# Kernel tuning notes

Measured on AMD Instinct MI355X. Metric: run time of the kernel, lower is better.

The kernel has to match this reference:

```python
import jax, jax.numpy as jnp
import numpy as np

N_NODES = 50000
N_EDGES = 800000
IN_DIM = 256
HID = 64
HEADS = 4
NUM_GRAPHS = 8
NEG_SLOPE = 0.2  # PyG GATConv default


def setup_inputs() -> dict:
    key = jax.random.key(0)
    ks = jax.random.split(key, 14)
    x = jax.random.normal(ks[0], (N_NODES, IN_DIM), jnp.float32)
    edge_index = jax.random.randint(ks[1], (2, N_EDGES), 0, N_NODES, jnp.int32)
    batch = jnp.sort(jax.random.randint(ks[2], (N_NODES,), 0, NUM_GRAPHS, jnp.int32))
    s1 = 1.0 / np.sqrt(IN_DIM)
    s2 = 1.0 / np.sqrt(HID * HEADS)
    W1 = jax.random.normal(ks[3], (IN_DIM, HEADS * HID), jnp.float32) * s1
    a_src1 = jax.random.normal(ks[4], (HEADS, HID), jnp.float32) * (1.0 / np.sqrt(HID))
    a_dst1 = jax.random.normal(ks[5], (HEADS, HID), jnp.float32) * (1.0 / np.sqrt(HID))
    b1 = jnp.zeros((HEADS * HID,), jnp.float32)
    W2 = jax.random.normal(ks[6], (HEADS * HID, HID), jnp.float32) * s2
    a_src2 = jax.random.normal(ks[7], (1, HID), jnp.float32) * (1.0 / np.sqrt(HID))
    a_dst2 = jax.random.normal(ks[8], (1, HID), jnp.float32) * (1.0 / np.sqrt(HID))
    b2 = jnp.zeros((HID,), jnp.float32)
    fcW = jax.random.normal(ks[9], (HID, 2), jnp.float32) * (1.0 / np.sqrt(HID))
    fcb = jnp.zeros((2,), jnp.float32)
    return {"x": x, "edge_index": edge_index, "batch": batch,
            "W1": W1, "a_src1": a_src1, "a_dst1": a_dst1, "b1": b1,
            "W2": W2, "a_src2": a_src2, "a_dst2": a_dst2, "b2": b2,
            "fcW": fcW, "fcb": fcb}


def _gat_layer(x, src, dst, W, a_src, a_dst, b, heads, out_dim, concat):
    """PyG-style GATConv: gather -> edge attention -> segment softmax -> scatter-add."""
    N = x.shape[0]
    xw = (x @ W).reshape(N, heads, out_dim)          # [N,H,C]
    al = jnp.einsum('nhc,hc->nh', xw, a_src)         # alpha_src per node
    ar = jnp.einsum('nhc,hc->nh', xw, a_dst)         # alpha_dst per node
    e = jax.nn.leaky_relu(al[src] + ar[dst], NEG_SLOPE)  # [E,H]
    m = jax.ops.segment_max(e, dst, num_segments=N)      # stable softmax per dst
    w = jnp.exp(e - m[dst])
    denom = jax.ops.segment_sum(w, dst, num_segments=N)
    alpha = w / denom[dst]                               # [E,H]
    out = jax.ops.segment_sum(alpha[:, :, None] * xw[src], dst, num_segments=N)  # [N,H,C]
    out = out.reshape(N, heads * out_dim) if concat else out.mean(axis=1)
    return out + b


def reference(x, edge_index, batch, W1, a_src1, a_dst1, b1, W2, a_src2, a_dst2, b2, fcW, fcb):
    N = x.shape[0]
    loops = jnp.arange(N, dtype=edge_index.dtype)  # PyG add_self_loops=True default
    src = jnp.concatenate([edge_index[0], loops])
    dst = jnp.concatenate([edge_index[1], loops])
    h = jax.nn.elu(_gat_layer(x, src, dst, W1, a_src1, a_dst1, b1, HEADS, HID, True))
    h = jax.nn.elu(_gat_layer(h, src, dst, W2, a_src2, a_dst2, b2, 1, HID, True))
    ssum = jax.ops.segment_sum(h, batch, num_segments=NUM_GRAPHS)
    cnt = jax.ops.segment_sum(jnp.ones((N, 1), h.dtype), batch, num_segments=NUM_GRAPHS)
    pooled = ssum / jnp.maximum(cnt, 1.0)  # global_mean_pool
    logits = pooled @ fcW + fcb
    return (h, logits)
```

## Files before the change

kernel.cpp:

```cpp
#include <hip/hip_runtime.h>

#define NEG_SLOPE 0.2f
#define NG 8
#define CH 64

typedef unsigned short ushort_t;
typedef __attribute__((ext_vector_type(8))) short short8v;
typedef __attribute__((ext_vector_type(4))) float f32x4;

__device__ __forceinline__ float lrelu(float x) { return x > 0.f ? x : NEG_SLOPE * x; }
__device__ __forceinline__ float eluf(float x) { return x > 0.f ? x : expm1f(x); }
__device__ __forceinline__ float wave_sum(float v) {
    #pragma unroll
    for (int o = 32; o; o >>= 1) v += __shfl_xor(v, o);
    return v;
}
__device__ __forceinline__ ushort_t f2bf(float f) {
    unsigned u = __float_as_uint(f);
    unsigned r = (u + 0x7FFFu + ((u >> 16) & 1u)) >> 16;
    return (ushort_t)r;
}
__device__ __forceinline__ float bf2f(ushort_t s) {
    return __uint_as_float(((unsigned)s) << 16);
}

__global__ __launch_bounds__(256) void k_hist(const int* __restrict__ ei,
                                              int* __restrict__ deg, int E) {
    int e = blockIdx.x * 256 + threadIdx.x;
    if (e < E) atomicAdd(&deg[ei[E + e]], 1);
}

__global__ __launch_bounds__(256) void k_scanA(const int* __restrict__ deg,
                                               int* __restrict__ bsum, int N) {
    __shared__ int wsums[4];
    int b = blockIdx.x, t = threadIdx.x;
    int base = b * 1024 + t * 4;
    int s = 0;
    #pragma unroll
    for (int k = 0; k < 4; k++) { int i = base + k; if (i < N) s += deg[i]; }
    #pragma unroll
    for (int o = 32; o; o >>= 1) s += __shfl_xor(s, o);
    if ((t & 63) == 0) wsums[t >> 6] = s;
    __syncthreads();
    if (t == 0) bsum[b] = wsums[0] + wsums[1] + wsums[2] + wsums[3];
}

__global__ __launch_bounds__(64) void k_scanB(const int* __restrict__ bsum,
                                              int* __restrict__ boff,
                                              int* __restrict__ rpN, int SB) {
    int lane = threadIdx.x;
    int own = (lane < SB) ? bsum[lane] : 0;
    int v = own;
    #pragma unroll
    for (int o = 1; o < 64; o <<= 1) { int y = __shfl_up(v, o); if (lane >= o) v += y; }
    if (lane < SB) boff[lane] = v - own;
    if (lane == 63) *rpN = v;
}

__global__ __launch_bounds__(256) void k_scanC(const int* __restrict__ deg,
                                               const int* __restrict__ boff,
                                               int* __restrict__ rp,
                                               int* __restrict__ cur, int N) {
    __shared__ int wtot[4];
    int b = blockIdx.x, t = threadIdx.x;
    int wid = t >> 6, lane = t & 63;
    int base = b * 1024 + t * 4;
    int d[4];
    #pragma unroll
    for (int k = 0; k < 4; k++) d[k] = (base + k < N) ? deg[base + k] : 0;
    int tsum = d[0] + d[1] + d[2] + d[3];
    int v = tsum;
    #pragma unroll
    for (int o = 1; o < 64; o <<= 1) { int y = __shfl_up(v, o); if (lane >= o) v += y; }
    if (lane == 63) wtot[wid] = v;
    __syncthreads();
    int wbase = 0;
    for (int k = 0; k < wid; k++) wbase += wtot[k];
    int run = boff[b] + wbase + v - tsum;
    #pragma unroll
    for (int k = 0; k < 4; k++) {
        if (base + k < N) { rp[base + k] = run; cur[base + k] = run; }
        run += d[k];
    }
}

__global__ __launch_bounds__(256) void k_fill(const int* __restrict__ ei,
                                              int* __restrict__ cur,
                                              int* __restrict__ csr, int E) {
    int e = blockIdx.x * 256 + threadIdx.x;
    if (e >= E) return;
    int s = ei[e], d = ei[E + e];
    int pos = atomicAdd(&cur[d], 1);
    csr[pos] = s;
}

__global__ __launch_bounds__(256) void k_w1t(const float* __restrict__ W1,
                                             ushort_t* __restrict__ w1th,
                                             ushort_t* __restrict__ w1tl) {
    int tile = blockIdx.x >> 3, ks = blockIdx.x & 7;
    for (int i = threadIdx.x; i < 512; i += 256) {
        int lane = i >> 3, e = i & 7;
        int jl = lane & 15, q = lane >> 4;
        int col = tile * 16 + jl;
        int k = ks * 32 + 8 * q + e;
        float w = W1[(size_t)k * 256 + col];
        ushort_t hi = f2bf(w);
        float lo = w - bf2f(hi);
        size_t o = (size_t)blockIdx.x * 512 + i;
        w1th[o] = hi;
        w1tl[o] = f2bf(lo);
    }
}

__global__ __launch_bounds__(256, 4) void k_gemm1(const float* __restrict__ x,
                                               const ushort_t* __restrict__ w1th,
                                               const ushort_t* __restrict__ w1tl,
                                               const float* __restrict__ a_s,
                                               const float* __restrict__ a_d,
                                               ushort_t* __restrict__ xw1b,
                                               float* __restrict__ al4,
                                               float* __restrict__ ar4, int N) {
    __shared__ __align__(16) unsigned char smem[33792];
    ushort_t* xh = (ushort_t*)smem;
    ushort_t* xl = (ushort_t*)(smem + 16896);
    int r0 = blockIdx.x * 32;
    int tid = threadIdx.x;
    int lane = tid & 63, wv = tid >> 6;
    for (int i = tid; i < 2048; i += 256) {
        int r = i >> 6, k4 = (i & 63) << 2;
        float4 v = (r0 + r < N) ? *(const float4*)(x + (size_t)(r0 + r) * 256 + k4)
                                : make_float4(0.f, 0.f, 0.f, 0.f);
        ushort4 h4, l4;
        h4.x = f2bf(v.x); l4.x = f2bf(v.x - bf2f(h4.x));
        h4.y = f2bf(v.y); l4.y = f2bf(v.y - bf2f(h4.y));
        h4.z = f2bf(v.z); l4.z = f2bf(v.z - bf2f(h4.z));
        h4.w = f2bf(v.w); l4.w = f2bf(v.w - bf2f(h4.w));
        *(ushort4*)(&xh[r * 264 + k4]) = h4;
        *(ushort4*)(&xl[r * 264 + k4]) = l4;
    }
    __syncthreads();
    int wr = wv & 1, wc = wv >> 1;
    int jl = lane & 15, q = lane >> 4;
    f32x4 acc[8];
    #pragma unroll
    for (int t = 0; t < 8; t++) acc[t] = (f32x4){0.f, 0.f, 0.f, 0.f};
    const ushort_t* xhp = &xh[(16 * wr + jl) * 264];
    const ushort_t* xlp = &xl[(16 * wr + jl) * 264];
    const ushort_t* bhb = w1th + (size_t)wc * 32768 + lane * 8;
    const ushort_t* blb = w1tl + (size_t)wc * 32768 + lane * 8;
    #pragma unroll 1
    for (int ks = 0; ks < 8; ks++) {
        int ko = 32 * ks + 8 * q;
        short8v ah = *(const short8v*)(xhp + ko);
        short8v alo = *(const short8v*)(xlp + ko);
        #pragma unroll
        for (int tp = 0; tp < 4; tp++) {
            int t0 = 2 * tp, t1 = 2 * tp + 1;
            short8v bh0 = *(const short8v*)(bhb + (t0 * 8 + ks) * 512);
            short8v bl0 = *(const short8v*)(blb + (t0 * 8 + ks) * 512);
            short8v bh1 = *(const short8v*)(bhb + (t1 * 8 + ks) * 512);
            short8v bl1 = *(const short8v*)(blb + (t1 * 8 + ks) * 512);
            acc[t0] = __builtin_amdgcn_mfma_f32_16x16x32_bf16(ah, bh0, acc[t0], 0, 0, 0);
            acc[t0] = __builtin_amdgcn_mfma_f32_16x16x32_bf16(ah, bl0, acc[t0], 0, 0, 0);
            acc[t0] = __builtin_amdgcn_mfma_f32_16x16x32_bf16(alo, bh0, acc[t0], 0, 0, 0);
            acc[t1] = __builtin_amdgcn_mfma_f32_16x16x32_bf16(ah, bh1, acc[t1], 0, 0, 0);
            acc[t1] = __builtin_amdgcn_mfma_f32_16x16x32_bf16(ah, bl1, acc[t1], 0, 0, 0);
            acc[t1] = __builtin_amdgcn_mfma_f32_16x16x32_bf16(alo, bh1, acc[t1], 0, 0, 0);
        }
    }
    __syncthreads();
    float* outb = (float*)smem;
    #pragma unroll
    for (int t = 0; t < 8; t++) {
        int c = 128 * wc + 16 * t + jl;
        int rb = 16 * wr + 4 * q;
        outb[(rb + 0) * 256 + c] = acc[t].x;
        outb[(rb + 1) * 256 + c] = acc[t].y;
        outb[(rb + 2) * 256 + c] = acc[t].z;
        outb[(rb + 3) * 256 + c] = acc[t].w;
    }
    __syncthreads();
    int c4 = lane << 2;
    int h = lane >> 4, kk = c4 & 63;
    float4 s4 = *(const float4*)(a_s + h * 64 + kk);
    float4 d4 = *(const float4*)(a_d + h * 64 + kk);
    float4 hv[8];
    #pragma unroll
    for (int t2 = 0; t2 < 8; t2++)
        hv[t2] = *(const float4*)(&outb[(wv + 4 * t2) * 256 + c4]);
    #pragma unroll
    for (int t2 = 0; t2 < 8; t2++) {
        float sl = hv[t2].x * s4.x + hv[t2].y * s4.y + hv[t2].z * s4.z + hv[t2].w * s4.w;
        float sr = hv[t2].x * d4.x + hv[t2].y * d4.y + hv[t2].z * d4.z + hv[t2].w * d4.w;
        #pragma unroll
        for (int o = 1; o < 16; o <<= 1) { sl += __shfl_xor(sl, o); sr += __shfl_xor(sr, o); }
        int r = r0 + wv + 4 * t2;
        if ((lane & 15) == 0 && r < N) {
            al4[(size_t)r * 4 + h] = sl;
            ar4[(size_t)r * 4 + h] = sr;
        }
    }
    __syncthreads();
    ushort_t* Ls = (ushort_t*)smem;
    #pragma unroll
    for (int t2 = 0; t2 < 8; t2++) {
        int rl = wv + 4 * t2;
        Ls[rl * 256 + (kk + 0) * 4 + h] = f2bf(hv[t2].x);
        Ls[rl * 256 + (kk + 1) * 4 + h] = f2bf(hv[t2].y);
        Ls[rl * 256 + (kk + 2) * 4 + h] = f2bf(hv[t2].z);
        Ls[rl * 256 + (kk + 3) * 4 + h] = f2bf(hv[t2].w);
    }
    __syncthreads();
    #pragma unroll
    for (int p = 0; p < 4; p++) {
        int flat = p * 2048 + tid * 8;
        int rl = flat >> 8, col = flat & 255;
        int r = r0 + rl;
        if (r < N)
            *(uint4*)(xw1b + (size_t)r * 256 + col) = *(const uint4*)(Ls + flat);
    }
}

__device__ __forceinline__ float4 wexp4(float4 a, float4 arn) {
    float4 w;
    w.x = __expf(lrelu(a.x + arn.x));
    w.y = __expf(lrelu(a.y + arn.y));
    w.z = __expf(lrelu(a.z + arn.z));
    w.w = __expf(lrelu(a.w + arn.w));
    return w;
}

__device__ __forceinline__ void gather1(int n, int lane,
                                        const int* __restrict__ rp,
                                        const int* __restrict__ csr,
                                        const float* __restrict__ al4,
                                        const float* __restrict__ ar4,
                                        const ushort_t* __restrict__ xw1b,
                                        const float* __restrict__ b1,
                                        float4* __restrict__ wb,
                                        int* __restrict__ sb,
                                        float* __restrict__ hrow) {
    int e0 = rp[n], e1 = rp[n + 1];
    float4 arn = *(const float4*)(ar4 + (size_t)n * 4);
    float4 aln = *(const float4*)(al4 + (size_t)n * 4);
    float4 wsf = wexp4(aln, arn);
    ushort4 sv = *(const ushort4*)(xw1b + (size_t)n * 256 + lane * 4);
    float a0 = wsf.x * bf2f(sv.x);
    float a1 = wsf.y * bf2f(sv.y);
    float a2 = wsf.z * bf2f(sv.z);
    float a3 = wsf.w * bf2f(sv.w);
    float px = 0.f, py = 0.f, pz = 0.f, pw = 0.f;
    for (int cs = e0; cs < e1; cs += CH) {
        int cnt = min(CH, e1 - cs);
        if (lane < cnt) {
            int s = csr[cs + lane];
            float4 A = *(const float4*)(al4 + (size_t)s * 4);
            float4 w = wexp4(A, arn);
            sb[lane] = s;
            wb[lane] = w;
            px += w.x; py += w.y; pz += w.z; pw += w.w;
        }
        asm volatile("s_waitcnt lgkmcnt(0)" ::: "memory");
        int jj = 0;
        for (; jj + 4 <= cnt; jj += 4) {
            int s0 = sb[jj],     s1 = sb[jj + 1];
            int s2 = sb[jj + 2], s3 = sb[jj + 3];
            float4 w0 = wb[jj],     w1 = wb[jj + 1];
            float4 w2 = wb[jj + 2], w3 = wb[jj + 3];
            ushort4 v0 = *(const ushort4*)(xw1b + (size_t)s0 * 256 + lane * 4);
            ushort4 v1 = *(const ushort4*)(xw1b + (size_t)s1 * 256 + lane * 4);
            ushort4 v2 = *(const ushort4*)(xw1b + (size_t)s2 * 256 + lane * 4);
            ushort4 v3 = *(const ushort4*)(xw1b + (size_t)s3 * 256 + lane * 4);
            a0 += w0.x * bf2f(v0.x) + w1.x * bf2f(v1.x) + w2.x * bf2f(v2.x) + w3.x * bf2f(v3.x);
            a1 += w0.y * bf2f(v0.y) + w1.y * bf2f(v1.y) + w2.y * bf2f(v2.y) + w3.y * bf2f(v3.y);
            a2 += w0.z * bf2f(v0.z) + w1.z * bf2f(v1.z) + w2.z * bf2f(v2.z) + w3.z * bf2f(v3.z);
            a3 += w0.w * bf2f(v0.w) + w1.w * bf2f(v1.w) + w2.w * bf2f(v2.w) + w3.w * bf2f(v3.w);
        }
        for (; jj < cnt; jj++) {
            int s = sb[jj];
            float4 w = wb[jj];
            ushort4 v = *(const ushort4*)(xw1b + (size_t)s * 256 + lane * 4);
            a0 += w.x * bf2f(v.x);
            a1 += w.y * bf2f(v.y);
            a2 += w.z * bf2f(v.z);
            a3 += w.w * bf2f(v.w);
        }
    }
    float wx = wave_sum(px) + wsf.x;
    float wy = wave_sum(py) + wsf.y;
    float wz = wave_sum(pz) + wsf.z;
    float ww = wave_sum(pw) + wsf.w;
    hrow[lane]       = eluf(a0 / wx + b1[lane]);
    hrow[64 + lane]  = eluf(a1 / wy + b1[64 + lane]);
    hrow[128 + lane] = eluf(a2 / wz + b1[128 + lane]);
    hrow[192 + lane] = eluf(a3 / ww + b1[192 + lane]);
}

__global__ __launch_bounds__(256, 8) void k_agg4(const int* __restrict__ rp,
                                                 const int* __restrict__ csr,
                                                 const float* __restrict__ al4,
                                                 const float* __restrict__ ar4,
                                                 const ushort_t* __restrict__ xw1b,
                                                 const float* __restrict__ b1,
                                                 const float* __restrict__ W2,
                                                 const float* __restrict__ as2,
                                                 const float* __restrict__ ad2,
                                                 ushort_t* __restrict__ xw2b,
                                                 float* __restrict__ al2,
                                                 float* __restrict__ ar2, int N) {
    __shared__ float hs[4][512];
    __shared__ float4 wbuf[4][CH];
    __shared__ int sbuf[4][CH];
    int wIdx = threadIdx.x >> 6;
    int w = (blockIdx.x * 256 + threadIdx.x) >> 6;
    int lane = threadIdx.x & 63;
    int nA = 2 * w, nB = 2 * w + 1;
    if (nA >= N) return;
    bool hasB = (nB < N);
    gather1(nA, lane, rp, csr, al4, ar4, xw1b, b1, wbuf[wIdx], sbuf[wIdx],
            &hs[wIdx][0]);
    if (hasB)
        gather1(nB, lane, rp, csr, al4, ar4, xw1b, b1, wbuf[wIdx], sbuf[wIdx],
                &hs[wIdx][256]);
    asm volatile("s_waitcnt lgkmcnt(0)" ::: "memory");
    {
        float accA = 0.f, accB = 0.f;
        const float* w2l = W2 + lane;
        #pragma unroll 2
        for (int k4 = 0; k4 < 64; k4++) {
            float u0 = w2l[(size_t)(k4 * 4 + 0) * 64];
            float u1 = w2l[(size_t)(k4 * 4 + 1) * 64];
            float u2 = w2l[(size_t)(k4 * 4 + 2) * 64];
            float u3 = w2l[(size_t)(k4 * 4 + 3) * 64];
            float4 hA = *(const float4*)(&hs[wIdx][k4 * 4]);
            accA += hA.x * u0 + hA.y * u1 + hA.z * u2 + hA.w * u3;
            if (hasB) {
                float4 hB = *(const float4*)(&hs[wIdx][256 + k4 * 4]);
                accB += hB.x * u0 + hB.y * u1 + hB.z * u2 + hB.w * u3;
            }
        }
        xw2b[(size_t)nA * 64 + lane] = f2bf(accA);
        float slA = wave_sum(accA * as2[lane]);
        float srA = wave_sum(accA * ad2[lane]);
        if (lane == 0) { al2[nA] = slA; ar2[nA] = srA; }
        if (hasB) {
            xw2b[(size_t)nB * 64 + lane] = f2bf(accB);
            float slB = wave_sum(accB * as2[lane]);
            float srB = wave_sum(accB * ad2[lane]);
            if (lane == 0) { al2[nB] = slB; ar2[nB] = srB; }
        }
    }
}

__global__ __launch_bounds__(256, 8) void k_agg2(const int* __restrict__ rp,
                                                 const int* __restrict__ csr,
                                                 const float* __restrict__ al2,
                                                 const float* __restrict__ ar2,
                                                 const ushort_t* __restrict__ xw2b,
                                                 const float* __restrict__ b2,
                                                 float* __restrict__ hout, int N) {
    __shared__ float wbuf[4][CH];
    __shared__ int sbuf[4][CH];
    int wIdx = threadIdx.x >> 6;
    int n = (blockIdx.x * 256 + threadIdx.x) >> 6;
    int lane = threadIdx.x & 63;
    if (n >= N) return;
    int e0 = rp[n], e1 = rp[n + 1];
    float arn = ar2[n];
    float wself = __expf(lrelu(al2[n] + arn));
    float acc = wself * bf2f(xw2b[(size_t)n * 64 + lane]);
    float p = 0.f;
    for (int cs = e0; cs < e1; cs += CH) {
        int cnt = min(CH, e1 - cs);
        if (lane < cnt) {
            int s = csr[cs + lane];
            float w = __expf(lrelu(al2[s] + arn));
            sbuf[wIdx][lane] = s;
            wbuf[wIdx][lane] = w;
            p += w;
        }
        asm volatile("s_waitcnt lgkmcnt(0)" ::: "memory");
        int jj = 0;
        for (; jj + 8 <= cnt; jj += 8) {
            int s0 = sbuf[wIdx][jj],     s1 = sbuf[wIdx][jj + 1];
            int s2 = sbuf[wIdx][jj + 2], s3 = sbuf[wIdx][jj + 3];
            int s4 = sbuf[wIdx][jj + 4], s5 = sbuf[wIdx][jj + 5];
            int s6 = sbuf[wIdx][jj + 6], s7 = sbuf[wIdx][jj + 7];
            float w0 = wbuf[wIdx][jj],     w1 = wbuf[wIdx][jj + 1];
            float w2 = wbuf[wIdx][jj + 2], w3 = wbuf[wIdx][jj + 3];
            float w4 = wbuf[wIdx][jj + 4], w5 = wbuf[wIdx][jj + 5];
            float w6 = wbuf[wIdx][jj + 6], w7 = wbuf[wIdx][jj + 7];
            float v0 = bf2f(xw2b[(size_t)s0 * 64 + lane]);
            float v1 = bf2f(xw2b[(size_t)s1 * 64 + lane]);
            float v2 = bf2f(xw2b[(size_t)s2 * 64 + lane]);
            float v3 = bf2f(xw2b[(size_t)s3 * 64 + lane]);
            float v4 = bf2f(xw2b[(size_t)s4 * 64 + lane]);
            float v5 = bf2f(xw2b[(size_t)s5 * 64 + lane]);
            float v6 = bf2f(xw2b[(size_t)s6 * 64 + lane]);
            float v7 = bf2f(xw2b[(size_t)s7 * 64 + lane]);
            acc += w0 * v0 + w1 * v1 + w2 * v2 + w3 * v3;
            acc += w4 * v4 + w5 * v5 + w6 * v6 + w7 * v7;
        }
        for (; jj + 4 <= cnt; jj += 4) {
            int s0 = sbuf[wIdx][jj],     s1 = sbuf[wIdx][jj + 1];
            int s2 = sbuf[wIdx][jj + 2], s3 = sbuf[wIdx][jj + 3];
            float w0 = wbuf[wIdx][jj],     w1 = wbuf[wIdx][jj + 1];
            float w2 = wbuf[wIdx][jj + 2], w3 = wbuf[wIdx][jj + 3];
            float v0 = bf2f(xw2b[(size_t)s0 * 64 + lane]);
            float v1 = bf2f(xw2b[(size_t)s1 * 64 + lane]);
            float v2 = bf2f(xw2b[(size_t)s2 * 64 + lane]);
            float v3 = bf2f(xw2b[(size_t)s3 * 64 + lane]);
            acc += w0 * v0 + w1 * v1 + w2 * v2 + w3 * v3;
        }
        for (; jj < cnt; jj++) {
            int s = sbuf[wIdx][jj];
            acc += wbuf[wIdx][jj] * bf2f(xw2b[(size_t)s * 64 + lane]);
        }
    }
    float wsum = wave_sum(p) + wself;
    hout[(size_t)n * 64 + lane] = eluf(acc / wsum + b2[lane]);
}

__global__ __launch_bounds__(256) void k_pool(const float* __restrict__ h2,
                                              const int* __restrict__ batch,
                                              float* __restrict__ pooled,
                                              float* __restrict__ cnt, int N) {
    int wave = (blockIdx.x * 256 + threadIdx.x) >> 6;
    int lane = threadIdx.x & 63;
    int n0 = wave * 32;
    if (n0 >= N) return;
    int n1 = min(n0 + 32, N);
    float acc = 0.f; int cl = 0;
    int curg = batch[n0];
    for (int n = n0; n < n1; n++) {
        int g = batch[n];
        if (g != curg) {
            atomicAdd(&pooled[curg * 64 + lane], acc);
            if (lane == 0) atomicAdd(&cnt[curg], (float)cl);
            acc = 0.f; cl = 0; curg = g;
        }
        acc += h2[(size_t)n * 64 + lane];
        cl++;
    }
    atomicAdd(&pooled[curg * 64 + lane], acc);
    if (lane == 0) atomicAdd(&cnt[curg], (float)cl);
}

__global__ __launch_bounds__(64) void k_logits(const float* __restrict__ pooled,
                                               const float* __restrict__ cnt,
                                               const float* __restrict__ fcW,
                                               const float* __restrict__ fcb,
                                               float* __restrict__ out) {
    int t = threadIdx.x;
    if (t >= NG * 2) return;
    int g = t >> 1, o = t & 1;
    float invc = 1.f / fmaxf(cnt[g], 1.f);
    float s = 0.f;
    for (int c = 0; c < 64; c++)
        s += pooled[g * 64 + c] * invc * fcW[c * 2 + o];
    s += fcb[o];
    out[g * 2 + o] = s;
}

extern "C" void kernel_launch(void* const* d_in, const int* in_sizes, int n_in,
                              void* d_out, int out_size, void* d_ws, size_t ws_size,
                              hipStream_t stream) {
    const float* x     = (const float*)d_in[0];
    const int*   ei    = (const int*)d_in[1];
    const int*   batch = (const int*)d_in[2];
    const float* W1    = (const float*)d_in[3];
    const float* as1   = (const float*)d_in[4];
    const float* ad1   = (const float*)d_in[5];
    const float* b1    = (const float*)d_in[6];
    const float* W2    = (const float*)d_in[7];
    const float* as2   = (const float*)d_in[8];
    const float* ad2   = (const float*)d_in[9];
    const float* b2v   = (const float*)d_in[10];
    const float* fcW   = (const float*)d_in[11];
    const float* fcb   = (const float*)d_in[12];
    float* out = (float*)d_out;

    const int N = in_sizes[2];
    const int E = in_sizes[1] / 2;
    const size_t nv  = (size_t)N * 64;
    const size_t nv4 = (size_t)N * 256;
    const int SB = (N + 1023) / 1024;

    ushort_t* xw1b = (ushort_t*)d_ws;
    ushort_t* xw2b   = xw1b + nv4;
    float*    al4    = (float*)(xw2b + nv);
    float*    ar4    = al4 + (size_t)N * 4;
    float*    al2    = ar4 + (size_t)N * 4;
    float*    ar2    = al2 + N;
    float*    pooled = ar2 + N;
    float*    cnt    = pooled + NG * 64;
    int*      deg    = (int*)(cnt + 8);
    int*      rp     = deg + N;
    int*      cur    = rp + N + 1;
    int*      csr    = cur + N;
    int*      bsum   = csr + E;
    int*      boff   = bsum + 64;
    ushort_t* w1th = (ushort_t*)(((uintptr_t)(boff + 64) + 255) & ~(uintptr_t)255);
    ushort_t* w1tl = w1th + 65536;

    const int gE  = (E + 255) / 256;
    const int gB4 = (N + 7) / 8;
    const int gB2 = (N + 3) / 4;
    const int gG1 = (N + 31) / 32;
    const int pw  = (N + 31) / 32;
    const int gP  = (pw * 64 + 255) / 256;

    hipMemsetAsync(deg, 0, (size_t)N * sizeof(int), stream);
    k_hist<<<gE, 256, 0, stream>>>(ei, deg, E);
    k_scanA<<<SB, 256, 0, stream>>>(deg, bsum, N);
    k_scanB<<<1, 64, 0, stream>>>(bsum, boff, rp + N, SB);
    k_scanC<<<SB, 256, 0, stream>>>(deg, boff, rp, cur, N);
    k_fill<<<gE, 256, 0, stream>>>(ei, cur, csr, E);
    k_w1t<<<128, 256, 0, stream>>>(W1, w1th, w1tl);

    k_gemm1<<<gG1, 256, 0, stream>>>(x, w1th, w1tl, as1, ad1, xw1b, al4, ar4, N);
    k_agg4<<<gB4, 256, 0, stream>>>(rp, csr, al4, ar4, xw1b, b1, W2, as2, ad2,
                                    xw2b, al2, ar2, N);

    k_agg2<<<gB2, 256, 0, stream>>>(rp, csr, al2, ar2, xw2b, b2v, out, N);

    hipMemsetAsync(pooled, 0, (NG * 64 + NG) * sizeof(float), stream);
    k_pool<<<gP, 256, 0, stream>>>(out, batch, pooled, cnt, N);
    k_logits<<<1, 64, 0, stream>>>(pooled, cnt, fcW, fcb, out + nv);
}
```

Baseline: 455.6 us.

## Restructure layer-2 aggregation to gather 8 edges per wave with 16-byte loads

The layer-2 aggregation kernel now splits each 64-lane wave into 8 groups of 8 lanes. Each group handles a different neighbor edge and loads a whole 16-byte chunk of 8 bf16 values, instead of each lane loading one 2-byte element per edge. Edge lists are padded to a multiple of 8 with zero-weight self entries. Partial sums are combined across groups with cross-lane shuffles at the end, and only 8 lanes write the output as float4 stores. This is meant to cut the number of memory instructions and raise the bytes fetched per load, at the cost of extra registers, a shuffle reduction and some wasted work on padded edges.

```diff
diff --git a/kernel.cpp b/kernel.cpp
--- a/kernel.cpp
+++ b/kernel.cpp
@@ -23,6 +23,14 @@
 __device__ __forceinline__ float bf2f(ushort_t s) {
     return __uint_as_float(((unsigned)s) << 16);
 }
+__device__ __forceinline__ float bfLO(unsigned u) { return __uint_as_float(u << 16); }
+__device__ __forceinline__ float bfHI(unsigned u) { return __uint_as_float(u & 0xFFFF0000u); }
+
+#define ACC8S(ww, vv)                                            \
+    a0 += (ww) * bfLO((vv).x); a1 += (ww) * bfHI((vv).x);        \
+    a2 += (ww) * bfLO((vv).y); a3 += (ww) * bfHI((vv).y);        \
+    a4 += (ww) * bfLO((vv).z); a5 += (ww) * bfHI((vv).z);        \
+    a6 += (ww) * bfLO((vv).w); a7 += (ww) * bfHI((vv).w);
 
 __global__ __launch_bounds__(256) void k_hist(const int* __restrict__ ei,
                                               int* __restrict__ deg, int E) {
@@ -368,57 +376,66 @@
     int e0 = rp[n], e1 = rp[n + 1];
     float arn = ar2[n];
     float wself = __expf(lrelu(al2[n] + arn));
-    float acc = wself * bf2f(xw2b[(size_t)n * 64 + lane]);
+    int g = lane >> 3, c8 = lane & 7;
+    float sm = (g == 0) ? wself : 0.f;
+    uint4 sv = *(const uint4*)(xw2b + (size_t)n * 64 + c8 * 8);
+    float a0 = sm * bfLO(sv.x), a1 = sm * bfHI(sv.x);
+    float a2 = sm * bfLO(sv.y), a3 = sm * bfHI(sv.y);
+    float a4 = sm * bfLO(sv.z), a5 = sm * bfHI(sv.z);
+    float a6 = sm * bfLO(sv.w), a7 = sm * bfHI(sv.w);
     float p = 0.f;
     for (int cs = e0; cs < e1; cs += CH) {
         int cnt = min(CH, e1 - cs);
+        int cnt8 = (cnt + 7) & ~7;
         if (lane < cnt) {
             int s = csr[cs + lane];
             float w = __expf(lrelu(al2[s] + arn));
             sbuf[wIdx][lane] = s;
             wbuf[wIdx][lane] = w;
             p += w;
+        } else if (lane < cnt8) {
+            sbuf[wIdx][lane] = n;
+            wbuf[wIdx][lane] = 0.f;
         }
         asm volatile("s_waitcnt lgkmcnt(0)" ::: "memory");
         int jj = 0;
-        for (; jj + 8 <= cnt; jj += 8) {
-            int s0 = sbuf[wIdx][jj],     s1 = sbuf[wIdx][jj + 1];
-            int s2 = sbuf[wIdx][jj + 2], s3 = sbuf[wIdx][jj + 3];
-            int s4 = sbuf[wIdx][jj + 4], s5 = sbuf[wIdx][jj + 5];
-            int s6 = sbuf[wIdx][jj + 6], s7 = sbuf[wIdx][jj + 7];
-            float w0 = wbuf[wIdx][jj],     w1 = wbuf[wIdx][jj + 1];
-            float w2 = wbuf[wIdx][jj + 2], w3 = wbuf[wIdx][jj + 3];
-            float w4 = wbuf[wIdx][jj + 4], w5 = wbuf[wIdx][jj + 5];
-            float w6 = wbuf[wIdx][jj + 6], w7 = wbuf[wIdx][jj + 7];
-            float v0 = bf2f(xw2b[(size_t)s0 * 64 + lane]);
-            float v1 = bf2f(xw2b[(size_t)s1 * 64 + lane]);
-            float v2 = bf2f(xw2b[(size_t)s2 * 64 + lane]);
-            float v3 = bf2f(xw2b[(size_t)s3 * 64 + lane]);
-            float v4 = bf2f(xw2b[(size_t)s4 * 64 + lane]);
-            float v5 = bf2f(xw2b[(size_t)s5 * 64 + lane]);
-            float v6 = bf2f(xw2b[(size_t)s6 * 64 + lane]);
-            float v7 = bf2f(xw2b[(size_t)s7 * 64 + lane]);
-            acc += w0 * v0 + w1 * v1 + w2 * v2 + w3 * v3;
-            acc += w4 * v4 + w5 * v5 + w6 * v6 + w7 * v7;
-        }
-        for (; jj + 4 <= cnt; jj += 4) {
-            int s0 = sbuf[wIdx][jj],     s1 = sbuf[wIdx][jj + 1];
-            int s2 = sbuf[wIdx][jj + 2], s3 = sbuf[wIdx][jj + 3];
-            float w0 = wbuf[wIdx][jj],     w1 = wbuf[wIdx][jj + 1];
-            float w2 = wbuf[wIdx][jj + 2], w3 = wbuf[wIdx][jj + 3];
-            float v0 = bf2f(xw2b[(size_t)s0 * 64 + lane]);
-            float v1 = bf2f(xw2b[(size_t)s1 * 64 + lane]);
-            float v2 = bf2f(xw2b[(size_t)s2 * 64 + lane]);
-            float v3 = bf2f(xw2b[(size_t)s3 * 64 + lane]);
-            acc += w0 * v0 + w1 * v1 + w2 * v2 + w3 * v3;
-        }
-        for (; jj < cnt; jj++) {
-            int s = sbuf[wIdx][jj];
-            acc += wbuf[wIdx][jj] * bf2f(xw2b[(size_t)s * 64 + lane]);
+        for (; jj + 16 <= cnt8; jj += 16) {
+            int s0 = sbuf[wIdx][jj + g], s1 = sbuf[wIdx][jj + 8 + g];
+            float w0 = wbuf[wIdx][jj + g], w1 = wbuf[wIdx][jj + 8 + g];
+            uint4 v0 = *(const uint4*)(xw2b + (size_t)s0 * 64 + c8 * 8);
+            uint4 v1 = *(const uint4*)(xw2b + (size_t)s1 * 64 + c8 * 8);
+            ACC8S(w0, v0);
+            ACC8S(w1, v1);
+        }
+        for (; jj < cnt8; jj += 8) {
+            int s0 = sbuf[wIdx][jj + g];
+            float w0 = wbuf[wIdx][jj + g];
+            uint4 v0 = *(const uint4*)(xw2b + (size_t)s0 * 64 + c8 * 8);
+            ACC8S(w0, v0);
         }
     }
     float wsum = wave_sum(p) + wself;
-    hout[(size_t)n * 64 + lane] = eluf(acc / wsum + b2[lane]);
+    a0 += __shfl_xor(a0, 8); a0 += __shfl_xor(a0, 16); a0 += __shfl_xor(a0, 32);
+    a1 += __shfl_xor(a1, 8); a1 += __shfl_xor(a1, 16); a1 += __shfl_xor(a1, 32);
+    a2 += __shfl_xor(a2, 8); a2 += __shfl_xor(a2, 16); a2 += __shfl_xor(a2, 32);
+    a3 += __shfl_xor(a3, 8); a3 += __shfl_xor(a3, 16); a3 += __shfl_xor(a3, 32);
+    a4 += __shfl_xor(a4, 8); a4 += __shfl_xor(a4, 16); a4 += __shfl_xor(a4, 32);
+    a5 += __shfl_xor(a5, 8); a5 += __shfl_xor(a5, 16); a5 += __shfl_xor(a5, 32);
+    a6 += __shfl_xor(a6, 8); a6 += __shfl_xor(a6, 16); a6 += __shfl_xor(a6, 32);
+    a7 += __shfl_xor(a7, 8); a7 += __shfl_xor(a7, 16); a7 += __shfl_xor(a7, 32);
+    if (lane < 8) {
+        float4 o0, o1;
+        o0.x = eluf(a0 / wsum + b2[lane * 8 + 0]);
+        o0.y = eluf(a1 / wsum + b2[lane * 8 + 1]);
+        o0.z = eluf(a2 / wsum + b2[lane * 8 + 2]);
+        o0.w = eluf(a3 / wsum + b2[lane * 8 + 3]);
+        o1.x = eluf(a4 / wsum + b2[lane * 8 + 4]);
+        o1.y = eluf(a5 / wsum + b2[lane * 8 + 5]);
+        o1.z = eluf(a6 / wsum + b2[lane * 8 + 6]);
+        o1.w = eluf(a7 / wsum + b2[lane * 8 + 7]);
+        *(float4*)(hout + (size_t)n * 64 + lane * 8) = o0;
+        *(float4*)(hout + (size_t)n * 64 + lane * 8 + 4) = o1;
+    }
 }
 
 __global__ __launch_bounds__(256) void k_pool(const float* __restrict__ h2,
```

Result: slower. 471.4 us (+3.5%).
